# Performance work log

Measured on AMD Instinct MI355X. Metric: run time of the kernel, lower is better.

## Reference

```python
import jax, jax.numpy as jnp
import numpy as np

B, S, H, D = 1, 8192, 16, 128
BS = 64            # sparse_block_size
NB = S // BS       # 128 blocks
NUM_ORACLES = 32
ORACLE = S // NUM_ORACLES          # 256
LOCAL = ORACLE // BS               # 4 sliding-window blocks
PATTERN_ID = 0


def _build_block_pattern():
    """Block-level mask exactly as DKernelPredefinedSparseAttention.create_mask((0,))."""
    qb = np.arange(NB)[:, None]
    kb = np.arange(NB)[None, :]
    causal = qb >= kb
    window = (qb - kb) < LOCAL
    vert = np.zeros(NB, dtype=bool)
    real_col = int(PATTERN_ID * ORACLE + 0.5)
    vert[real_col // BS:(real_col + ORACLE) // BS] = True
    vert[0:1] = True
    mask = causal & (window | vert[None, :])
    kmax = int(mask.sum(axis=1).max())  # = 8 for this pattern
    kidx = np.zeros((NB, kmax), dtype=np.int32)
    kvalid = np.zeros((NB, kmax), dtype=bool)
    for i in range(NB):
        idx = np.nonzero(mask[i])[0]
        kidx[i, :len(idx)] = idx
        kvalid[i, :len(idx)] = True
    return kidx, kvalid


def setup_inputs() -> dict:
    key = jax.random.key(0)
    kq, kk, kv = jax.random.split(key, 3)
    q = jax.random.normal(kq, (B, S, H, D), dtype=jnp.float32)
    k = jax.random.normal(kk, (B, S, H, D), dtype=jnp.float32)
    v = jax.random.normal(kv, (B, S, H, D), dtype=jnp.float32)
    kidx_np, kvalid_np = _build_block_pattern()
    return {"q": q, "k": k, "v": v,
            "kidx": jnp.asarray(kidx_np), "kvalid": jnp.asarray(kvalid_np)}


def reference(q, k, v, kidx, kvalid):
    # q,k,v: [B,S,H,D] (bshd). kidx/kvalid: [NB, Kmax] active k-block ids per q-block.
    b, s, h, d = q.shape
    nb = s // BS
    kmax = kidx.shape[1]
    qb = q.reshape(b, nb, BS, h, d)
    kb = k.reshape(b, nb, BS, h, d)
    vb = v.reshape(b, nb, BS, h, d)
    # Gather only active k/v blocks -> [B, nb, Kmax, BS, H, D]
    kg = kb[:, kidx]
    vg = vb[:, kidx]
    scale = 1.0 / jnp.sqrt(jnp.float32(d))
    # [B, H, nb, BS(q), Kmax, BS(k)]
    scores = jnp.einsum('bqahd,bqkchd->bhqakc', qb, kg) * scale
    # element-level causal mask within the block pattern
    qpos = jnp.arange(nb)[:, None] * BS + jnp.arange(BS)[None, :]          # [nb, BS]
    kpos = kidx[..., None] * BS + jnp.arange(BS)[None, None, :]            # [nb, Kmax, BS]
    allow = (qpos[:, :, None, None] >= kpos[:, None, :, :]) & kvalid[:, None, :, None]
    scores = jnp.where(allow[None, None], scores, jnp.float32(-1e30))
    probs = jax.nn.softmax(scores.reshape(b, h, nb, BS, kmax * BS), axis=-1)
    probs = probs.reshape(scores.shape)
    out = jnp.einsum('bhqakc,bqkchd->bqahd', probs, vg)
    return out.reshape(b, s, h, d)
```

## Files before the change

kernel.cpp:

```cpp
#include <hip/hip_runtime.h>
#include <hip/hip_bf16.h>

#define HH 16
#define DD 128
#define NBQ 128
#define SS 8192

typedef __attribute__((ext_vector_type(4))) float f32x4;
typedef __attribute__((ext_vector_type(4))) short bf16x4;
typedef __attribute__((ext_vector_type(8))) short bf16x8;

__device__ __forceinline__ short f2bf_hw(float f) {
  __hip_bfloat16 b = __float2bfloat16(f);
  return __builtin_bit_cast(short, b);
}

__device__ __forceinline__ void gload_lds16(const void* g, void* l) {
  __builtin_amdgcn_global_load_lds(
      (const __attribute__((address_space(1))) void*)g,
      (__attribute__((address_space(3))) void*)l, 16, 0, 0);
}

__global__ __launch_bounds__(256)
void conv_k_kernel(const float* __restrict__ kg, unsigned short* __restrict__ kb) {
  const size_t e = ((size_t)blockIdx.x * 256 + threadIdx.x) * 4;
  const int h = (int)(e >> 20);
  const int s = (int)((e >> 7) & (SS - 1));
  const int d = (int)(e & 127);
  f32x4 a = *(const f32x4*)(kg + ((size_t)s * HH + h) * DD + d);
  bf16x4 o;
  o[0] = f2bf_hw(a[0]); o[1] = f2bf_hw(a[1]);
  o[2] = f2bf_hw(a[2]); o[3] = f2bf_hw(a[3]);
  *(bf16x4*)(kb + e) = o;
}

__global__ __launch_bounds__(256)
void conv_vt2_kernel(const float* __restrict__ vg, unsigned short* __restrict__ vt) {
  __shared__ unsigned short tile[128 * 72];
  const int kb = blockIdx.x, h = blockIdx.y, tid = threadIdx.x;
  {
    const int r = tid >> 2, q = tid & 3;
    const float* vp = vg + ((size_t)(kb * 64 + r) * HH + h) * DD + q * 32;
    #pragma unroll
    for (int c = 0; c < 8; ++c) {
      f32x4 a = *(const f32x4*)(vp + c * 4);
      #pragma unroll
      for (int j = 0; j < 4; ++j)
        tile[(q * 32 + c * 4 + j) * 72 + r] = (unsigned short)f2bf_hw(a[j]);
    }
  }
  __syncthreads();
  const int d = tid >> 1, half = tid & 1;
  unsigned short* op = vt + ((size_t)(h * NBQ + kb) * 128 + d) * 64 + half * 32;
  #pragma unroll
  for (int j = 0; j < 4; ++j) {
    bf16x8 f;
    #pragma unroll
    for (int e = 0; e < 8; ++e) {
      const int p = half * 32 + j * 8 + e;
      const int key = ((p >> 2) & 3) * 16 + (p >> 4) * 4 + (p & 3);
      f[e] = (short)tile[d * 72 + key];
    }
    *(bf16x8*)(op + j * 8) = f;
  }
}

#define SWK(o) ((o) ^ ((((o) >> 8) & 7) << 4))
#define SWV(o) ((o) ^ ((((o) >> 7) & 7) << 4))

__global__ __launch_bounds__(256, 2)
void sparse_attn_v12(const float* __restrict__ qg_, const unsigned short* __restrict__ kbuf,
                     const unsigned short* __restrict__ vtbuf, float* __restrict__ outg) {
  extern __shared__ __align__(16) char lds[];

  const int qgrp = blockIdx.x;
  const int h    = blockIdx.y;
  const int tid  = threadIdx.x;
  const int wid  = tid >> 6;
  const int lane = tid & 63;
  const int l15  = lane & 15;
  const int lg   = lane >> 4;

  const int qlo  = qgrp * 2, qhi = qgrp * 2 + 1;
  const int qb_w = qlo + (wid >> 1);
  const int rib0 = (wid & 1) * 32;

  const int nv     = (qhi + 1 < 4) ? qhi + 1 : 4;
  const int wstart = (qlo - 3 > 4) ? qlo - 3 : 4;
  const int nw     = (qhi - wstart + 1 > 0) ? qhi - wstart + 1 : 0;
  const int nlist  = nv + nw;

  const float scale = 0.12752030522080552f;

  bf16x8 qa[2][4];
  #pragma unroll
  for (int m = 0; m < 2; ++m) {
    const float* qp = qg_ + ((size_t)(qgrp * 128 + wid * 32 + m * 16 + l15) * HH + h) * DD;
    #pragma unroll
    for (int kc = 0; kc < 4; ++kc) {
      const int d0 = kc * 32 + lg * 8;
      f32x4 a = *(const f32x4*)(qp + d0);
      f32x4 b = *(const f32x4*)(qp + d0 + 4);
      bf16x8 f;
      f[0] = f2bf_hw(a[0] * scale); f[1] = f2bf_hw(a[1] * scale);
      f[2] = f2bf_hw(a[2] * scale); f[3] = f2bf_hw(a[3] * scale);
      f[4] = f2bf_hw(b[0] * scale); f[5] = f2bf_hw(b[1] * scale);
      f[6] = f2bf_hw(b[2] * scale); f[7] = f2bf_hw(b[3] * scale);
      qa[m][kc] = f;
    }
  }

  f32x4 oa[2][8];
  #pragma unroll
  for (int m = 0; m < 2; ++m)
    #pragma unroll
    for (int i = 0; i < 8; ++i) oa[m][i] = (f32x4){0.f, 0.f, 0.f, 0.f};
  float mr[2] = {-1e30f, -1e30f};
  float lr[2] = {0.f, 0.f};

  const char* kbase = (const char*)kbuf + ((size_t)h * NBQ << 14);
  const char* vbase = (const char*)vtbuf + ((size_t)h * NBQ << 14);

  {
    #pragma unroll
    for (int p = 0; p < 4; ++p) {
      const int ob = p * 4096 + wid * 1024;
      const int o  = ob + lane * 16;
      gload_lds16(kbase + SWK(o), lds + ob);
      gload_lds16(vbase + SWV(o), lds + 16384 + ob);
    }
  }
  __syncthreads();

  for (int t = 0; t < nlist; ++t) {
    const int kb = (t < nv) ? t : (wstart + (t - nv));
    const bool valid = (kb <= qb_w) && ((qb_w - kb < 4) || (kb < 4));
    char* Vb = lds + 16384 + (t & 1) * 16384;

    f32x4 s[2][4];
    if (valid) {
      #pragma unroll
      for (int m = 0; m < 2; ++m)
        #pragma unroll
        for (int kt = 0; kt < 4; ++kt) s[m][kt] = (f32x4){0.f, 0.f, 0.f, 0.f};
      __builtin_amdgcn_s_setprio(1);
      #pragma unroll
      for (int kt = 0; kt < 4; ++kt) {
        const int key = kt * 16 + l15;
        #pragma unroll
        for (int kc = 0; kc < 4; ++kc) {
          const int off = (key * 256 + (kc * 32 + lg * 8) * 2) ^ ((key & 7) << 4);
          bf16x8 kf = *(const bf16x8*)(lds + off);
          s[0][kt] = __builtin_amdgcn_mfma_f32_16x16x32_bf16(kf, qa[0][kc], s[0][kt], 0, 0, 0);
          s[1][kt] = __builtin_amdgcn_mfma_f32_16x16x32_bf16(kf, qa[1][kc], s[1][kt], 0, 0, 0);
        }
      }
      __builtin_amdgcn_s_setprio(0);
    }

    __syncthreads();

    if (t + 1 < nlist) {
      const int kbn = (t + 1 < nv) ? (t + 1) : (wstart + (t + 1 - nv));
      const char* ksrc = kbase + ((size_t)kbn << 14);
      const char* vsrc = vbase + ((size_t)kbn << 14);
      char* Vd = lds + 16384 + ((t + 1) & 1) * 16384;
      #pragma unroll
      for (int p = 0; p < 4; ++p) {
        const int ob = p * 4096 + wid * 1024;
        const int o  = ob + lane * 16;
        gload_lds16(ksrc + SWK(o), lds + ob);
        gload_lds16(vsrc + SWV(o), Vd + ob);
      }
    }

    if (valid) {
      if (kb == qb_w) {
        #pragma unroll
        for (int m = 0; m < 2; ++m) {
          const int rib = rib0 + m * 16 + l15;
          #pragma unroll
          for (int kt = 0; kt < 4; ++kt)
            #pragma unroll
            for (int r = 0; r < 4; ++r) {
              const int key = kt * 16 + lg * 4 + r;
              if (rib < key) s[m][kt][r] = -1e30f;
            }
        }
      }

      #pragma unroll
      for (int m = 0; m < 2; ++m) {
        float a0 = fmaxf(fmaxf(s[m][0][0], s[m][0][1]), fmaxf(s[m][0][2], s[m][0][3]));
        float a1 = fmaxf(fmaxf(s[m][1][0], s[m][1][1]), fmaxf(s[m][1][2], s[m][1][3]));
        float a2 = fmaxf(fmaxf(s[m][2][0], s[m][2][1]), fmaxf(s[m][2][2], s[m][2][3]));
        float a3 = fmaxf(fmaxf(s[m][3][0], s[m][3][1]), fmaxf(s[m][3][2], s[m][3][3]));
        float lanemax = fmaxf(fmaxf(a0, a1), fmaxf(a2, a3));
        if (!__all(lanemax <= mr[m] + 8.f)) {
          float mx = lanemax;
          mx = fmaxf(mx, __shfl_xor(mx, 16));
          mx = fmaxf(mx, __shfl_xor(mx, 32));
          const float mnew = fmaxf(mr[m], mx);
          const float sc = __builtin_amdgcn_exp2f(mr[m] - mnew);
          lr[m] *= sc;
          mr[m] = mnew;
          const float s0 = __shfl(sc, lg * 4 + 0);
          const float s1 = __shfl(sc, lg * 4 + 1);
          const float s2 = __shfl(sc, lg * 4 + 2);
          const float s3 = __shfl(sc, lg * 4 + 3);
          #pragma unroll
          for (int nd = 0; nd < 8; ++nd) {
            oa[m][nd][0] *= s0; oa[m][nd][1] *= s1;
            oa[m][nd][2] *= s2; oa[m][nd][3] *= s3;
          }
        }
        float lsum = 0.f;
        #pragma unroll
        for (int kt = 0; kt < 4; ++kt)
          #pragma unroll
          for (int r = 0; r < 4; ++r) {
            const float p = __builtin_amdgcn_exp2f(s[m][kt][r] - mr[m]);
            s[m][kt][r] = p;
            lsum += p;
          }
        lr[m] += lsum;
      }

      bf16x4 pa[2][4];
      #pragma unroll
      for (int m = 0; m < 2; ++m)
        #pragma unroll
        for (int kt = 0; kt < 4; ++kt) {
          unsigned u0 = (unsigned)(unsigned short)f2bf_hw(s[m][kt][0]) |
                        ((unsigned)(unsigned short)f2bf_hw(s[m][kt][1]) << 16);
          unsigned u1 = (unsigned)(unsigned short)f2bf_hw(s[m][kt][2]) |
                        ((unsigned)(unsigned short)f2bf_hw(s[m][kt][3]) << 16);
          uint2 uu; uu.x = u0; uu.y = u1;
          pa[m][kt] = __builtin_bit_cast(bf16x4, uu);
        }

      __builtin_amdgcn_s_setprio(1);
      #pragma unroll
      for (int nd = 0; nd < 8; ++nd) {
        const int d = nd * 16 + l15;
        #pragma unroll
        for (int hb = 0; hb < 2; ++hb) {
          const int off = (d * 128 + lg * 32 + hb * 16) ^ ((d & 7) << 4);
          bf16x8 v2 = *(const bf16x8*)(Vb + off);
          bf16x4 vlo = __builtin_shufflevector(v2, v2, 0, 1, 2, 3);
          bf16x4 vhi = __builtin_shufflevector(v2, v2, 4, 5, 6, 7);
          oa[0][nd] = __builtin_amdgcn_mfma_f32_16x16x16bf16_1k(pa[0][2 * hb],     vlo, oa[0][nd], 0, 0, 0);
          oa[1][nd] = __builtin_amdgcn_mfma_f32_16x16x16bf16_1k(pa[1][2 * hb],     vlo, oa[1][nd], 0, 0, 0);
          oa[0][nd] = __builtin_amdgcn_mfma_f32_16x16x16bf16_1k(pa[0][2 * hb + 1], vhi, oa[0][nd], 0, 0, 0);
          oa[1][nd] = __builtin_amdgcn_mfma_f32_16x16x16bf16_1k(pa[1][2 * hb + 1], vhi, oa[1][nd], 0, 0, 0);
        }
      }
      __builtin_amdgcn_s_setprio(0);
    }
    __syncthreads();
  }

  #pragma unroll
  for (int m = 0; m < 2; ++m) {
    float l = lr[m];
    l += __shfl_xor(l, 16);
    l += __shfl_xor(l, 32);
    const float inv = 1.0f / l;
    const float i0 = __shfl(inv, lg * 4 + 0);
    const float i1 = __shfl(inv, lg * 4 + 1);
    const float i2 = __shfl(inv, lg * 4 + 2);
    const float i3 = __shfl(inv, lg * 4 + 3);
    float* op = outg + ((size_t)(qgrp * 128 + wid * 32 + m * 16) * HH + h) * DD;
    #pragma unroll
    for (int nd = 0; nd < 8; ++nd) {
      const int d = nd * 16 + l15;
      op[(size_t)(lg * 4 + 0) * HH * DD + d] = oa[m][nd][0] * i0;
      op[(size_t)(lg * 4 + 1) * HH * DD + d] = oa[m][nd][1] * i1;
      op[(size_t)(lg * 4 + 2) * HH * DD + d] = oa[m][nd][2] * i2;
      op[(size_t)(lg * 4 + 3) * HH * DD + d] = oa[m][nd][3] * i3;
    }
  }
}

extern "C" void kernel_launch(void* const* d_in, const int* in_sizes, int n_in,
                              void* d_out, int out_size, void* d_ws, size_t ws_size,
                              hipStream_t stream) {
  const float* q = (const float*)d_in[0];
  const float* k = (const float*)d_in[1];
  const float* v = (const float*)d_in[2];
  float* out = (float*)d_out;
  const size_t elems = (size_t)HH * SS * DD;
  unsigned short* kbuf  = (unsigned short*)d_ws;
  unsigned short* vtbuf = kbuf + elems;

  conv_k_kernel<<<(int)(elems / 4 / 256), 256, 0, stream>>>(k, kbuf);
  conv_vt2_kernel<<<dim3(NBQ, HH), 256, 0, stream>>>(v, vtbuf);
  sparse_attn_v12<<<dim3(NBQ / 2, HH), 256, 49152, stream>>>(q, kbuf, vtbuf, out);
}
```

Measured before the change: 113.5 us.

## Use 8 waves per block with one 16-row tile each, prefetch V earlier

The attention kernel now launches 512 threads (8 waves) per block instead of 256, and each wave owns a single 16-row query tile rather than two. This halves per-wave accumulator and Q registers and doubles the waves available to hide latency. The next V block's async load is also issued before the QK^T MFMAs rather than after the barrier, so it overlaps more compute. The tradeoff is fewer MFMAs per LDS K/V fragment read, since each fragment is no longer reused across two query tiles, and more waves contending on the block barriers.

```diff
diff --git a/kernel.cpp b/kernel.cpp
--- a/kernel.cpp
+++ b/kernel.cpp
@@ -68,8 +68,8 @@
 #define SWK(o) ((o) ^ ((((o) >> 8) & 7) << 4))
 #define SWV(o) ((o) ^ ((((o) >> 7) & 7) << 4))
 
-__global__ __launch_bounds__(256, 2)
-void sparse_attn_v12(const float* __restrict__ qg_, const unsigned short* __restrict__ kbuf,
+__global__ __launch_bounds__(512, 4)
+void sparse_attn_v13(const float* __restrict__ qg_, const unsigned short* __restrict__ kbuf,
                      const unsigned short* __restrict__ vtbuf, float* __restrict__ outg) {
   extern __shared__ __align__(16) char lds[];
 
@@ -82,8 +82,8 @@
   const int lg   = lane >> 4;
 
   const int qlo  = qgrp * 2, qhi = qgrp * 2 + 1;
-  const int qb_w = qlo + (wid >> 1);
-  const int rib0 = (wid & 1) * 32;
+  const int qb_w = qlo + (wid >> 2);
+  const int rib0 = (wid & 3) * 16;
 
   const int nv     = (qhi + 1 < 4) ? qhi + 1 : 4;
   const int wstart = (qlo - 3 > 4) ? qlo - 3 : 4;
@@ -92,10 +92,11 @@
 
   const float scale = 0.12752030522080552f;
 
-  bf16x8 qa[2][4];
-  #pragma unroll
-  for (int m = 0; m < 2; ++m) {
-    const float* qp = qg_ + ((size_t)(qgrp * 128 + wid * 32 + m * 16 + l15) * HH + h) * DD;
+  const int rowg = qgrp * 128 + (wid >> 2) * 64 + rib0;
+
+  bf16x8 qa[4];
+  {
+    const float* qp = qg_ + ((size_t)(rowg + l15) * HH + h) * DD;
     #pragma unroll
     for (int kc = 0; kc < 4; ++kc) {
       const int d0 = kc * 32 + lg * 8;
@@ -106,25 +107,23 @@
       f[2] = f2bf_hw(a[2] * scale); f[3] = f2bf_hw(a[3] * scale);
       f[4] = f2bf_hw(b[0] * scale); f[5] = f2bf_hw(b[1] * scale);
       f[6] = f2bf_hw(b[2] * scale); f[7] = f2bf_hw(b[3] * scale);
-      qa[m][kc] = f;
-    }
-  }
-
-  f32x4 oa[2][8];
+      qa[kc] = f;
+    }
+  }
+
+  f32x4 oa[8];
   #pragma unroll
-  for (int m = 0; m < 2; ++m)
-    #pragma unroll
-    for (int i = 0; i < 8; ++i) oa[m][i] = (f32x4){0.f, 0.f, 0.f, 0.f};
-  float mr[2] = {-1e30f, -1e30f};
-  float lr[2] = {0.f, 0.f};
+  for (int i = 0; i < 8; ++i) oa[i] = (f32x4){0.f, 0.f, 0.f, 0.f};
+  float mr = -1e30f;
+  float lr = 0.f;
 
   const char* kbase = (const char*)kbuf + ((size_t)h * NBQ << 14);
   const char* vbase = (const char*)vtbuf + ((size_t)h * NBQ << 14);
 
   {
     #pragma unroll
-    for (int p = 0; p < 4; ++p) {
-      const int ob = p * 4096 + wid * 1024;
+    for (int p = 0; p < 2; ++p) {
+      const int ob = p * 8192 + wid * 1024;
       const int o  = ob + lane * 16;
       gload_lds16(kbase + SWK(o), lds + ob);
       gload_lds16(vbase + SWV(o), lds + 16384 + ob);
@@ -136,13 +135,24 @@
     const int kb = (t < nv) ? t : (wstart + (t - nv));
     const bool valid = (kb <= qb_w) && ((qb_w - kb < 4) || (kb < 4));
     char* Vb = lds + 16384 + (t & 1) * 16384;
-
-    f32x4 s[2][4];
+    const bool havenext = (t + 1 < nlist);
+    const int kbn = havenext ? ((t + 1 < nv) ? (t + 1) : (wstart + (t + 1 - nv))) : 0;
+
+    if (havenext) {
+      const char* vsrc = vbase + ((size_t)kbn << 14);
+      char* Vd = lds + 16384 + ((t + 1) & 1) * 16384;
+      #pragma unroll
+      for (int p = 0; p < 2; ++p) {
+        const int ob = p * 8192 + wid * 1024;
+        const int o  = ob + lane * 16;
+        gload_lds16(vsrc + SWV(o), Vd + ob);
+      }
+    }
+
+    f32x4 s[4];
     if (valid) {
       #pragma unroll
-      for (int m = 0; m < 2; ++m)
-        #pragma unroll
-        for (int kt = 0; kt < 4; ++kt) s[m][kt] = (f32x4){0.f, 0.f, 0.f, 0.f};
+      for (int kt = 0; kt < 4; ++kt) s[kt] = (f32x4){0.f, 0.f, 0.f, 0.f};
       __builtin_amdgcn_s_setprio(1);
       #pragma unroll
       for (int kt = 0; kt < 4; ++kt) {
@@ -151,8 +161,7 @@
         for (int kc = 0; kc < 4; ++kc) {
           const int off = (key * 256 + (kc * 32 + lg * 8) * 2) ^ ((key & 7) << 4);
           bf16x8 kf = *(const bf16x8*)(lds + off);
-          s[0][kt] = __builtin_amdgcn_mfma_f32_16x16x32_bf16(kf, qa[0][kc], s[0][kt], 0, 0, 0);
-          s[1][kt] = __builtin_amdgcn_mfma_f32_16x16x32_bf16(kf, qa[1][kc], s[1][kt], 0, 0, 0);
+          s[kt] = __builtin_amdgcn_mfma_f32_16x16x32_bf16(kf, qa[kc], s[kt], 0, 0, 0);
         }
       }
       __builtin_amdgcn_s_setprio(0);
@@ -160,58 +169,50 @@
 
     __syncthreads();
 
-    if (t + 1 < nlist) {
-      const int kbn = (t + 1 < nv) ? (t + 1) : (wstart + (t + 1 - nv));
+    if (havenext) {
       const char* ksrc = kbase + ((size_t)kbn << 14);
-      const char* vsrc = vbase + ((size_t)kbn << 14);
-      char* Vd = lds + 16384 + ((t + 1) & 1) * 16384;
-      #pragma unroll
-      for (int p = 0; p < 4; ++p) {
-        const int ob = p * 4096 + wid * 1024;
+      #pragma unroll
+      for (int p = 0; p < 2; ++p) {
+        const int ob = p * 8192 + wid * 1024;
         const int o  = ob + lane * 16;
         gload_lds16(ksrc + SWK(o), lds + ob);
-        gload_lds16(vsrc + SWV(o), Vd + ob);
       }
     }
 
     if (valid) {
       if (kb == qb_w) {
-        #pragma unroll
-        for (int m = 0; m < 2; ++m) {
-          const int rib = rib0 + m * 16 + l15;
+        const int rib = rib0 + l15;
+        #pragma unroll
+        for (int kt = 0; kt < 4; ++kt)
           #pragma unroll
-          for (int kt = 0; kt < 4; ++kt)
-            #pragma unroll
-            for (int r = 0; r < 4; ++r) {
-              const int key = kt * 16 + lg * 4 + r;
-              if (rib < key) s[m][kt][r] = -1e30f;
-            }
-        }
-      }
-
-      #pragma unroll
-      for (int m = 0; m < 2; ++m) {
-        float a0 = fmaxf(fmaxf(s[m][0][0], s[m][0][1]), fmaxf(s[m][0][2], s[m][0][3]));
-        float a1 = fmaxf(fmaxf(s[m][1][0], s[m][1][1]), fmaxf(s[m][1][2], s[m][1][3]));
-        float a2 = fmaxf(fmaxf(s[m][2][0], s[m][2][1]), fmaxf(s[m][2][2], s[m][2][3]));
-        float a3 = fmaxf(fmaxf(s[m][3][0], s[m][3][1]), fmaxf(s[m][3][2], s[m][3][3]));
+          for (int r = 0; r < 4; ++r) {
+            const int key = kt * 16 + lg * 4 + r;
+            if (rib < key) s[kt][r] = -1e30f;
+          }
+      }
+
+      {
+        float a0 = fmaxf(fmaxf(s[0][0], s[0][1]), fmaxf(s[0][2], s[0][3]));
+        float a1 = fmaxf(fmaxf(s[1][0], s[1][1]), fmaxf(s[1][2], s[1][3]));
+        float a2 = fmaxf(fmaxf(s[2][0], s[2][1]), fmaxf(s[2][2], s[2][3]));
+        float a3 = fmaxf(fmaxf(s[3][0], s[3][1]), fmaxf(s[3][2], s[3][3]));
         float lanemax = fmaxf(fmaxf(a0, a1), fmaxf(a2, a3));
-        if (!__all(lanemax <= mr[m] + 8.f)) {
+        if (!__all(lanemax <= mr + 8.f)) {
           float mx = lanemax;
           mx = fmaxf(mx, __shfl_xor(mx, 16));
           mx = fmaxf(mx, __shfl_xor(mx, 32));
-          const float mnew = fmaxf(mr[m], mx);
-          const float sc = __builtin_amdgcn_exp2f(mr[m] - mnew);
-          lr[m] *= sc;
-          mr[m] = mnew;
+          const float mnew = fmaxf(mr, mx);
+          const float sc = __builtin_amdgcn_exp2f(mr - mnew);
+          lr *= sc;
+          mr = mnew;
           const float s0 = __shfl(sc, lg * 4 + 0);
           const float s1 = __shfl(sc, lg * 4 + 1);
           const float s2 = __shfl(sc, lg * 4 + 2);
           const float s3 = __shfl(sc, lg * 4 + 3);
           #pragma unroll
           for (int nd = 0; nd < 8; ++nd) {
-            oa[m][nd][0] *= s0; oa[m][nd][1] *= s1;
-            oa[m][nd][2] *= s2; oa[m][nd][3] *= s3;
+            oa[nd][0] *= s0; oa[nd][1] *= s1;
+            oa[nd][2] *= s2; oa[nd][3] *= s3;
           }
         }
         float lsum = 0.f;
@@ -219,25 +220,23 @@
         for (int kt = 0; kt < 4; ++kt)
           #pragma unroll
           for (int r = 0; r < 4; ++r) {
-            const float p = __builtin_amdgcn_exp2f(s[m][kt][r] - mr[m]);
-            s[m][kt][r] = p;
+            const float p = __builtin_amdgcn_exp2f(s[kt][r] - mr);
+            s[kt][r] = p;
             lsum += p;
           }
-        lr[m] += lsum;
-      }
-
-      bf16x4 pa[2][4];
-      #pragma unroll
-      for (int m = 0; m < 2; ++m)
-        #pragma unroll
-        for (int kt = 0; kt < 4; ++kt) {
-          unsigned u0 = (unsigned)(unsigned short)f2bf_hw(s[m][kt][0]) |
-                        ((unsigned)(unsigned short)f2bf_hw(s[m][kt][1]) << 16);
-          unsigned u1 = (unsigned)(unsigned short)f2bf_hw(s[m][kt][2]) |
-                        ((unsigned)(unsigned short)f2bf_hw(s[m][kt][3]) << 16);
-          uint2 uu; uu.x = u0; uu.y = u1;
-          pa[m][kt] = __builtin_bit_cast(bf16x4, uu);
-        }
+        lr += lsum;
+      }
+
+      bf16x4 pa[4];
+      #pragma unroll
+      for (int kt = 0; kt < 4; ++kt) {
+        unsigned u0 = (unsigned)(unsigned short)f2bf_hw(s[kt][0]) |
+                      ((unsigned)(unsigned short)f2bf_hw(s[kt][1]) << 16);
+        unsigned u1 = (unsigned)(unsigned short)f2bf_hw(s[kt][2]) |
+                      ((unsigned)(unsigned short)f2bf_hw(s[kt][3]) << 16);
+        uint2 uu; uu.x = u0; uu.y = u1;
+        pa[kt] = __builtin_bit_cast(bf16x4, uu);
+      }
 
       __builtin_amdgcn_s_setprio(1);
       #pragma unroll
@@ -249,10 +248,8 @@
           bf16x8 v2 = *(const bf16x8*)(Vb + off);
           bf16x4 vlo = __builtin_shufflevector(v2, v2, 0, 1, 2, 3);
           bf16x4 vhi = __builtin_shufflevector(v2, v2, 4, 5, 6, 7);
-          oa[0][nd] = __builtin_amdgcn_mfma_f32_16x16x16bf16_1k(pa[0][2 * hb],     vlo, oa[0][nd], 0, 0, 0);
-          oa[1][nd] = __builtin_amdgcn_mfma_f32_16x16x16bf16_1k(pa[1][2 * hb],     vlo, oa[1][nd], 0, 0, 0);
-          oa[0][nd] = __builtin_amdgcn_mfma_f32_16x16x16bf16_1k(pa[0][2 * hb + 1], vhi, oa[0][nd], 0, 0, 0);
-          oa[1][nd] = __builtin_amdgcn_mfma_f32_16x16x16bf16_1k(pa[1][2 * hb + 1], vhi, oa[1][nd], 0, 0, 0);
+          oa[nd] = __builtin_amdgcn_mfma_f32_16x16x16bf16_1k(pa[2 * hb],     vlo, oa[nd], 0, 0, 0);
+          oa[nd] = __builtin_amdgcn_mfma_f32_16x16x16bf16_1k(pa[2 * hb + 1], vhi, oa[nd], 0, 0, 0);
         }
       }
       __builtin_amdgcn_s_setprio(0);
@@ -260,9 +257,8 @@
     __syncthreads();
   }
 
-  #pragma unroll
-  for (int m = 0; m < 2; ++m) {
-    float l = lr[m];
+  {
+    float l = lr;
     l += __shfl_xor(l, 16);
     l += __shfl_xor(l, 32);
     const float inv = 1.0f / l;
@@ -270,14 +266,14 @@
     const float i1 = __shfl(inv, lg * 4 + 1);
     const float i2 = __shfl(inv, lg * 4 + 2);
     const float i3 = __shfl(inv, lg * 4 + 3);
-    float* op = outg + ((size_t)(qgrp * 128 + wid * 32 + m * 16) * HH + h) * DD;
+    float* op = outg + ((size_t)rowg * HH + h) * DD;
     #pragma unroll
     for (int nd = 0; nd < 8; ++nd) {
       const int d = nd * 16 + l15;
-      op[(size_t)(lg * 4 + 0) * HH * DD + d] = oa[m][nd][0] * i0;
-      op[(size_t)(lg * 4 + 1) * HH * DD + d] = oa[m][nd][1] * i1;
-      op[(size_t)(lg * 4 + 2) * HH * DD + d] = oa[m][nd][2] * i2;
-      op[(size_t)(lg * 4 + 3) * HH * DD + d] = oa[m][nd][3] * i3;
+      op[(size_t)(lg * 4 + 0) * HH * DD + d] = oa[nd][0] * i0;
+      op[(size_t)(lg * 4 + 1) * HH * DD + d] = oa[nd][1] * i1;
+      op[(size_t)(lg * 4 + 2) * HH * DD + d] = oa[nd][2] * i2;
+      op[(size_t)(lg * 4 + 3) * HH * DD + d] = oa[nd][3] * i3;
     }
   }
 }
@@ -295,5 +291,5 @@
 
   conv_k_kernel<<<(int)(elems / 4 / 256), 256, 0, stream>>>(k, kbuf);
   conv_vt2_kernel<<<dim3(NBQ, HH), 256, 0, stream>>>(v, vtbuf);
-  sparse_attn_v12<<<dim3(NBQ / 2, HH), 256, 49152, stream>>>(q, kbuf, vtbuf, out);
-}
+  sparse_attn_v13<<<dim3(NBQ / 2, HH), 512, 49152, stream>>>(q, kbuf, vtbuf, out);
+}
```

Measured after the change: 114.8 us. No clear change (+1.1%).
